# Optimization experiments

Hardware: AMD Instinct MI355X
Metric: run time of the kernel (lower is better)

## Reference

```python
import jax, jax.numpy as jnp
import numpy as np

WS = 5   # window_size
VN = 8   # view_num -> H = W = VN*WS = 40


def _layernorm(x, g, b, eps=1e-5):
    mu = x.mean(-1, keepdims=True)
    var = ((x - mu) ** 2).mean(-1, keepdims=True)
    return (x - mu) * jax.lax.rsqrt(var + eps) * g + b


def _rel_index():
    # standard Swin relative-position index for a WS x WS window
    coords = np.stack(np.meshgrid(np.arange(WS), np.arange(WS), indexing='ij')).reshape(2, -1)
    rel = (coords[:, :, None] - coords[:, None, :]).transpose(1, 2, 0)  # (T,T,2)
    rel = rel + (WS - 1)
    return rel[:, :, 0] * (2 * WS - 1) + rel[:, :, 1]  # (T,T) int


def _attn_mask(H, W):
    # checkerboard mask: outer product of flattened per-window checkerboard,
    # 0 where both positions are 'on', -100 elsewhere (matches masked_fill logic)
    ckbd = np.zeros((H, W), np.float32)
    ckbd[0::2, 1::2] = 1.0
    ckbd[1::2, 0::2] = 1.0
    win = ckbd.reshape(VN, WS, VN, WS).transpose(0, 2, 1, 3).reshape(VN * VN, WS * WS)
    m = win[:, :, None] * win[:, None, :]  # (N,T,T)
    return np.where(m == 0.0, -100.0, 0.0).astype(np.float32)


def setup_inputs() -> dict:
    key = jax.random.key(0)
    ks = jax.random.split(key, 8)
    B, C, H, W = 64, 256, 40, 40
    nh = 8
    dim2 = 2 * C
    hid = int(dim2 * 2.0)

    def n(k, shape, s=0.02):
        return jax.random.normal(k, shape, jnp.float32) * s

    return dict(
        x=jax.random.normal(ks[0], (B, C, H, W), jnp.float32),
        qkv_w=n(ks[1], (C, 3 * C)), qkv_b=jnp.zeros((3 * C,), jnp.float32),
        rel_table=n(ks[2], ((2 * WS - 1) ** 2, nh)),
        proj_w=n(ks[3], (C, dim2)), proj_b=jnp.zeros((dim2,), jnp.float32),
        mlp_w1=n(ks[4], (dim2, hid)), mlp_b1=jnp.zeros((hid,), jnp.float32),
        mlp_w2=n(ks[5], (hid, dim2)), mlp_b2=jnp.zeros((dim2,), jnp.float32),
        norm1_g=jnp.ones((C,), jnp.float32), norm1_b=jnp.zeros((C,), jnp.float32),
        norm2_g=jnp.ones((dim2,), jnp.float32), norm2_b=jnp.zeros((dim2,), jnp.float32),
    )


def reference(x, qkv_w, qkv_b, rel_table, proj_w, proj_b,
              mlp_w1, mlp_b1, mlp_w2, mlp_b2,
              norm1_g, norm1_b, norm2_g, norm2_b):
    B, C, H, W = x.shape
    nh = rel_table.shape[1]
    hd = C // nh
    N = VN * VN           # windows
    T = WS * WS           # tokens per window
    scale = hd ** -0.5

    xs = _layernorm(x.reshape(B, C, H * W).transpose(0, 2, 1), norm1_g, norm1_b)  # (B,L,C)
    qkv = xs @ qkv_w + qkv_b                                   # (B,L,3C)
    qkv = qkv.reshape(B, H, W, 3, C).transpose(3, 0, 4, 1, 2)  # (3,B,C,H,W)
    # windowize: (3,B,C,u,ws,v,ws) -> (3,B,N,C,T)
    qkv = qkv.reshape(3, B, C, VN, WS, VN, WS).transpose(0, 1, 3, 5, 2, 4, 6).reshape(3, B, N, C, T)
    # NOTE: original splits C as (head_dim, num_heads) -- head index is MINOR
    qkv = qkv.reshape(3, B, N, hd, nh, T).transpose(0, 1, 2, 4, 5, 3)  # (3,B,N,nh,T,hd)
    q, k, v = qkv[0] * scale, qkv[1], qkv[2]

    attn = jnp.einsum('bnhtd,bnhsd->bnhts', q, k)              # (B,N,nh,T,T)
    bias = rel_table[jnp.asarray(_rel_index())].transpose(2, 0, 1)  # (nh,T,T)
    mask = jnp.asarray(_attn_mask(H, W))                       # (N,T,T)
    attn = jax.nn.softmax(attn + bias[None, None] + mask[None, :, None], axis=-1)

    out = jnp.einsum('bnhts,bnhsd->bnhtd', attn, v)            # (B,N,nh,T,hd)
    out = out.reshape(B, N, nh, WS, WS, hd).transpose(0, 1, 3, 4, 2, 5)  # (B,N,ws,ws,nh,hd)
    # 'B (u v) h w nh c -> B (u h v w) (nh c)'
    out = out.reshape(B, VN, VN, WS, WS, C).transpose(0, 1, 3, 2, 4, 5).reshape(B, H * W, C)

    y = out @ proj_w + proj_b                                  # (B,L,2C)
    h = _layernorm(y, norm2_g, norm2_b)
    h = jax.nn.gelu(h @ mlp_w1 + mlp_b1, approximate=False) @ mlp_w2 + mlp_b2
    y = y + h
    return y.transpose(0, 2, 1).reshape(B, -1, H, W)           # (B,2C,H,W)
```

## Files before the change

### kernel.cpp

```cpp
#include <hip/hip_runtime.h>
#include <math.h>

#define B_   64
#define C_   256
#define L_   1600
#define T_   25
#define ROWS (B_*L_)
#define QSCALE 0.17677669529663687f

typedef _Float16 f16;
typedef f16 f16x8 __attribute__((ext_vector_type(8)));
typedef f16 f16x4 __attribute__((ext_vector_type(4)));
typedef f16 f16x2 __attribute__((ext_vector_type(2)));
typedef float f32x4 __attribute__((ext_vector_type(4)));

__device__ __forceinline__ void gload_lds16(const void* g, void* l) {
  __builtin_amdgcn_global_load_lds(
      (const __attribute__((address_space(1))) unsigned int*)g,
      (__attribute__((address_space(3))) unsigned int*)l, 16, 0, 0);
}

__device__ __forceinline__ float dot8(f16x8 a, f16x8 b, float acc) {
  union U { f16x8 v; f16x2 p[4]; };
  U ua; ua.v = a;
  U ub; ub.v = b;
#pragma unroll
  for (int i = 0; i < 4; ++i)
    acc = __builtin_amdgcn_fdot2(ua.p[i], ub.p[i], acc, false);
  return acc;
}

__global__ __launch_bounds__(256) void wtrans(const float* __restrict__ w,
                                              f16* __restrict__ o, int K, int N) {
  __shared__ f16 tile[64][72];
  int tid = threadIdx.x;
  int n0 = blockIdx.x * 64, k0 = blockIdx.y * 64;
  int nn = tid & 63, kq = tid >> 6;
#pragma unroll
  for (int i = 0; i < 16; ++i) {
    int k = kq * 16 + i;
    tile[nn][k] = (f16)w[(size_t)(k0 + k) * N + n0 + nn];
  }
  __syncthreads();
#pragma unroll
  for (int jj = 0; jj < 2; ++jj) {
    int e = jj * 256 + tid;
    int nr = e >> 3, kb = e & 7;
    *(f16x8*)&o[(size_t)(n0 + nr) * K + k0 + kb * 8] = *(const f16x8*)&tile[nr][kb * 8];
  }
}

__global__ __launch_bounds__(256) void ln1_fused(const float* __restrict__ x,
    const float* __restrict__ g, const float* __restrict__ be,
    f16* __restrict__ xs) {
  __shared__ float t32[256][65];
  __shared__ float gL[256], beL[256];
  int tid = threadIdx.x;
  gL[tid] = g[tid]; beL[tid] = be[tid];
  int r0 = blockIdx.x * 64;
  int w = tid >> 6, rl = tid & 63;
  int grow = r0 + rl;
  int b = grow / L_, l = grow - b * L_;
  const float* xb = x + (size_t)b * (C_ * L_) + l;
#pragma unroll
  for (int i = 0; i < 64; ++i) {
    int c = w + i * 4;
    t32[c][rl] = xb[(size_t)c * L_];
  }
  __syncthreads();
  int row = tid >> 2, q = tid & 3;
  float s = 0.f, s2 = 0.f;
#pragma unroll
  for (int i = 0; i < 64; ++i) {
    float vv = t32[q * 64 + i][row];
    s += vv; s2 += vv * vv;
  }
  s += __shfl_xor(s, 1); s2 += __shfl_xor(s2, 1);
  s += __shfl_xor(s, 2); s2 += __shfl_xor(s2, 2);
  float m = s * (1.0f / 256.0f);
  float rr = rsqrtf(s2 * (1.0f / 256.0f) - m * m + 1e-5f);
  f16* orow = &xs[(size_t)(r0 + row) * 256 + q * 64];
#pragma unroll
  for (int z8 = 0; z8 < 8; ++z8) {
    f16x8 ov;
#pragma unroll
    for (int z = 0; z < 8; ++z) {
      int c = q * 64 + z8 * 8 + z;
      ov[z] = (f16)((t32[c][row] - m) * rr * gL[c] + beL[c]);
    }
    *(f16x8*)(orow + z8 * 8) = ov;
  }
}

template<int K, int N, int EPI, int NCB>
__global__ __launch_bounds__(256) void gemm16(
    const f16* __restrict__ A, const f16* __restrict__ BT,
    const float* __restrict__ bias,
    float* __restrict__ outF, f16* __restrict__ outH,
    const f16* __restrict__ resid, int row_off, int nrp8) {
  __shared__ f16 As[2][128 * 32];
  __shared__ f16 Bs[2][128 * 32];
  int tid = threadIdx.x;
  int w = tid >> 6, lane = tid & 63;
  int wr = w >> 1, wc = w & 1;
  int bid = blockIdx.x;
  int xcd = bid & 7, j1d = bid >> 3;
  int member = j1d % NCB, grp = j1d / NCB;
  int r0 = (xcd * nrp8 + grp) * 128;
  int n0 = member * 128;

  f32x4 acc[4][4] = {};

  int srow0 = w * 16 + (lane >> 2);
  int st4 = lane & 3;

  const int NT = K / 32;

#define STAGE_T(kt, buf)                                                      \
  {                                                                           \
    int k0s = (kt) * 32;                                                      \
    _Pragma("unroll")                                                         \
    for (int i = 0; i < 2; ++i) {                                             \
      int row = i * 64 + srow0;                                               \
      int cb = st4 ^ ((row >> 1) & 3);                                        \
      gload_lds16(A + (size_t)(r0 + row) * K + k0s + cb * 8,                  \
                  &As[buf][(i * 4 + w) * 512]);                               \
    }                                                                         \
    _Pragma("unroll")                                                         \
    for (int i = 0; i < 2; ++i) {                                             \
      int row = i * 64 + srow0;                                               \
      int cb = st4 ^ ((row >> 1) & 3);                                        \
      gload_lds16(BT + (size_t)(n0 + row) * K + k0s + cb * 8,                 \
                  &Bs[buf][(i * 4 + w) * 512]);                               \
    }                                                                         \
  }

#define COMPUTE_T(buf)                                                        \
  {                                                                           \
    f16x8 af[4], bf[4];                                                       \
    _Pragma("unroll")                                                         \
    for (int m = 0; m < 4; ++m) {                                             \
      int ar = wr * 64 + m * 16 + (lane & 15);                                \
      int sl = (lane >> 4) ^ ((ar >> 1) & 3);                                 \
      af[m] = *(const f16x8*)&As[buf][ar * 32 + sl * 8];                      \
    }                                                                         \
    _Pragma("unroll")                                                         \
    for (int n = 0; n < 4; ++n) {                                             \
      int br = wc * 64 + n * 16 + (lane & 15);                                \
      int sl = (lane >> 4) ^ ((br >> 1) & 3);                                 \
      bf[n] = *(const f16x8*)&Bs[buf][br * 32 + sl * 8];                      \
    }                                                                         \
    _Pragma("unroll")                                                         \
    for (int m = 0; m < 4; ++m)                                               \
      _Pragma("unroll")                                                       \
      for (int n = 0; n < 4; ++n)                                             \
        acc[m][n] =                                                           \
            __builtin_amdgcn_mfma_f32_16x16x32_f16(af[m], bf[n], acc[m][n],   \
                                                   0, 0, 0);                  \
  }

  STAGE_T(0, 0);
  asm volatile("s_waitcnt vmcnt(0)" ::: "memory");
  __builtin_amdgcn_s_barrier();

  int cur = 0;
#pragma unroll 2
  for (int t = 0; t < NT - 1; ++t) {
    STAGE_T(t + 1, cur ^ 1);
    COMPUTE_T(cur);
    asm volatile("s_waitcnt vmcnt(0) lgkmcnt(0)" ::: "memory");
    __builtin_amdgcn_s_barrier();
    cur ^= 1;
  }
  COMPUTE_T(cur);

#undef STAGE_T
#undef COMPUTE_T

  if constexpr (EPI != 3) {
#pragma unroll
    for (int m = 0; m < 4; ++m) {
#pragma unroll
      for (int n = 0; n < 4; ++n) {
        int gcol = n0 + wc * 64 + n * 16 + (lane & 15);
        float bb = bias[gcol];
#pragma unroll
        for (int j = 0; j < 4; ++j) {
          int grow = r0 + wr * 64 + m * 16 + ((lane >> 4) << 2) + j;
          float vv = acc[m][n][j] + bb;
          if constexpr (EPI == 0) {
            outH[(size_t)grow * N + gcol] = (f16)vv;
          } else {
            float gl = 0.5f * vv * (1.0f + erff(vv * 0.70710678118654752f));
            outH[(size_t)grow * N + gcol] = (f16)gl;
          }
        }
      }
    }
  } else {
#pragma unroll
    for (int m = 0; m < 4; ++m) {
      int growl = r0 + wr * 64 + m * 16 + ((lane >> 4) << 2);
      int growg = row_off + growl;
      int b = growg / L_;
      int l = growg - b * L_;
#pragma unroll
      for (int n = 0; n < 4; ++n) {
        int gcol = n0 + wc * 64 + n * 16 + (lane & 15);
        float bb = bias[gcol];
        float4 o;
        o.x = acc[m][n][0] + bb + (float)resid[(size_t)(growg + 0) * 512 + gcol];
        o.y = acc[m][n][1] + bb + (float)resid[(size_t)(growg + 1) * 512 + gcol];
        o.z = acc[m][n][2] + bb + (float)resid[(size_t)(growg + 2) * 512 + gcol];
        o.w = acc[m][n][3] + bb + (float)resid[(size_t)(growg + 3) * 512 + gcol];
        *(float4*)&outF[((size_t)b * 512 + gcol) * L_ + l] = o;
      }
    }
  }
}

#define PST 776
__global__ __launch_bounds__(256) void attn_kernel(const f16* __restrict__ qkv,
                                                   const float* __restrict__ rel,
                                                   f16* __restrict__ outp) {
  __shared__ f16 qc[T_][PST];
  __shared__ f16 relL[81 * 8];
  int tid = threadIdx.x;
  int bn = blockIdx.x;
  int b = bn >> 6, n = bn & 63;
  int u = n >> 3, v = n & 7;

  for (int e = tid; e < 648; e += 256) relL[e] = (f16)rel[e];

  for (int e = tid; e < T_ * 96; e += 256) {
    int t = e / 96;
    int g = e - t * 96;
    int i = t / 5, j = t - i * 5;
    int l = (u * 5 + i) * 40 + v * 5 + j;
    f16x8 val = *(const f16x8*)&qkv[(size_t)(b * L_ + l) * 768 + g * 8];
    int which = g >> 5;
    int d = g & 31;
    int base = which * 256 + d;
#pragma unroll
    for (int h = 0; h < 8; ++h)
      qc[t][base + h * 32] = val[h];
  }
  __syncthreads();

  int h = tid >> 5, t = tid & 31;
  if (t < T_) {
    int i1 = t / 5, j1 = t - i1 * 5;
    int par1 = (u + v + i1 + j1) & 1;
    const f16* qp = &qc[t][h * 32];
    f16x8 q0 = *(const f16x8*)(qp + 0);
    f16x8 q1 = *(const f16x8*)(qp + 8);
    f16x8 q2 = *(const f16x8*)(qp + 16);
    f16x8 q3 = *(const f16x8*)(qp + 24);

    float p[T_];
    float mx = -1e30f;
#pragma unroll
    for (int s = 0; s < T_; ++s) {
      int i2 = s / 5, j2 = s - i2 * 5;
      const f16* kp = &qc[s][256 + h * 32];
      f16x8 k0 = *(const f16x8*)(kp + 0);
      f16x8 k1 = *(const f16x8*)(kp + 8);
      f16x8 k2 = *(const f16x8*)(kp + 16);
      f16x8 k3 = *(const f16x8*)(kp + 24);
      float d0 = 0.f, d1 = 0.f;
      d0 = dot8(q0, k0, d0);
      d1 = dot8(q1, k1, d1);
      d0 = dot8(q2, k2, d0);
      d1 = dot8(q3, k3, d1);
      float bias = (float)relL[((i1 - i2 + 4) * 9 + (j1 - j2 + 4)) * 8 + h];
      int par2 = (u + v + i2 + j2) & 1;
      float sc = (d0 + d1) * QSCALE + bias + ((par1 & par2) ? 0.0f : -100.0f);
      p[s] = sc;
      mx = fmaxf(mx, sc);
    }
    float sum = 0.f;
#pragma unroll
    for (int s = 0; s < T_; ++s) {
      float e = __expf(p[s] - mx);
      p[s] = e;
      sum += e;
    }
    float inv = 1.0f / sum;
#pragma unroll
    for (int s = 0; s < T_; ++s) p[s] *= inv;

    int l = (u * 5 + i1) * 40 + v * 5 + j1;
    f16* op = &outp[(size_t)(b * L_ + l) * 256 + h * 32];

#pragma unroll
    for (int half = 0; half < 2; ++half) {
      float acc[16] = {};
#pragma unroll
      for (int s = 0; s < T_; ++s) {
        const f16* vp = &qc[s][512 + h * 32 + half * 16];
        f16x8 v0 = *(const f16x8*)(vp + 0);
        f16x8 v1 = *(const f16x8*)(vp + 8);
        float ps = p[s];
#pragma unroll
        for (int z = 0; z < 8; ++z) {
          acc[z]     += ps * (float)v0[z];
          acc[8 + z] += ps * (float)v1[z];
        }
      }
#pragma unroll
      for (int z8 = 0; z8 < 2; ++z8) {
        f16x8 ov;
#pragma unroll
        for (int z = 0; z < 8; ++z) ov[z] = (f16)acc[z8 * 8 + z];
        *(f16x8*)(op + half * 16 + z8 * 8) = ov;
      }
    }
  }
}

__global__ __launch_bounds__(256) void ln2_fused(const f16* __restrict__ y,
    const float* __restrict__ g, const float* __restrict__ be,
    f16* __restrict__ yln) {
  int wv = threadIdx.x >> 6, lane = threadIdx.x & 63;
  int row = blockIdx.x * 4 + wv;
  const f16x8* yp = (const f16x8*)(y + (size_t)row * 512);
  f16x8 h0 = yp[lane];
  float v[8];
  float s = 0.f, s2 = 0.f;
#pragma unroll
  for (int z = 0; z < 8; ++z) {
    v[z] = (float)h0[z];
    s += v[z]; s2 += v[z] * v[z];
  }
#pragma unroll
  for (int o = 32; o; o >>= 1) { s += __shfl_xor(s, o); s2 += __shfl_xor(s2, o); }
  float m = s * (1.0f / 512.0f);
  float rr = rsqrtf(s2 * (1.0f / 512.0f) - m * m + 1e-5f);
  float4 g0 = ((const float4*)g)[lane * 2], g1 = ((const float4*)g)[lane * 2 + 1];
  float4 b0 = ((const float4*)be)[lane * 2], b1 = ((const float4*)be)[lane * 2 + 1];
  float gg[8] = {g0.x, g0.y, g0.z, g0.w, g1.x, g1.y, g1.z, g1.w};
  float bb[8] = {b0.x, b0.y, b0.z, b0.w, b1.x, b1.y, b1.z, b1.w};
  f16x8 o8;
#pragma unroll
  for (int z = 0; z < 8; ++z)
    o8[z] = (f16)((v[z] - m) * rr * gg[z] + bb[z]);
  *(f16x8*)&yln[(size_t)row * 512 + lane * 8] = o8;
}

extern "C" void kernel_launch(void* const* d_in, const int* in_sizes, int n_in,
                              void* d_out, int out_size, void* d_ws, size_t ws_size,
                              hipStream_t stream) {
  const float* x      = (const float*)d_in[0];
  const float* qkv_w  = (const float*)d_in[1];
  const float* qkv_b  = (const float*)d_in[2];
  const float* rel    = (const float*)d_in[3];
  const float* proj_w = (const float*)d_in[4];
  const float* proj_b = (const float*)d_in[5];
  const float* w1     = (const float*)d_in[6];
  const float* b1     = (const float*)d_in[7];
  const float* w2     = (const float*)d_in[8];
  const float* b2     = (const float*)d_in[9];
  const float* g1     = (const float*)d_in[10];
  const float* be1    = (const float*)d_in[11];
  const float* g2     = (const float*)d_in[12];
  const float* be2    = (const float*)d_in[13];
  float* out = (float*)d_out;

  char* w8 = (char*)d_ws;
  f16* qkv_wT  = (f16*)(w8 + 1638400);
  f16* proj_wT = qkv_wT + 768 * 256;
  f16* w1T     = proj_wT + 512 * 256;
  f16* w2T     = w1T + 1024 * 512;
  char* P0 = w8 + 4390912;
  f16* qkv_h = (f16*)P0;
  f16* y_h   = (f16*)P0;
  char* P1 = P0 + (size_t)ROWS * 768 * 2;
  f16* xs_h  = (f16*)P1;
  f16* att_h = (f16*)(P1 + (size_t)ROWS * 256 * 2);
  f16* yln   = (f16*)P1;
  char* P2 = P1 + (size_t)ROWS * 512 * 2;
  f16* hid = (f16*)P2;

  size_t need_full = 4390912 + (size_t)ROWS * 768 * 2 + (size_t)ROWS * 512 * 2
                   + (size_t)ROWS * 1024 * 2;
  bool full = ws_size >= need_full;

  wtrans<<<dim3(768 / 64, 256 / 64), 256, 0, stream>>>(qkv_w, qkv_wT, 256, 768);
  wtrans<<<dim3(512 / 64, 256 / 64), 256, 0, stream>>>(proj_w, proj_wT, 256, 512);
  wtrans<<<dim3(1024 / 64, 512 / 64), 256, 0, stream>>>(w1, w1T, 512, 1024);
  wtrans<<<dim3(512 / 64, 1024 / 64), 256, 0, stream>>>(w2, w2T, 1024, 512);

  ln1_fused<<<ROWS / 64, 256, 0, stream>>>(x, g1, be1, xs_h);

  gemm16<256, 768, 0, 6><<<6 * (ROWS / 128), 256, 0, stream>>>(
      xs_h, qkv_wT, qkv_b, nullptr, qkv_h, nullptr, 0, (ROWS / 128) / 8);

  attn_kernel<<<B_ * 64, 256, 0, stream>>>(qkv_h, rel, att_h);

  gemm16<256, 512, 0, 4><<<4 * (ROWS / 128), 256, 0, stream>>>(
      att_h, proj_wT, proj_b, nullptr, y_h, nullptr, 0, (ROWS / 128) / 8);

  ln2_fused<<<ROWS / 4, 256, 0, stream>>>(y_h, g2, be2, yln);

  if (full) {
    gemm16<512, 1024, 2, 8><<<8 * (ROWS / 128), 256, 0, stream>>>(
        yln, w1T, b1, nullptr, hid, nullptr, 0, (ROWS / 128) / 8);
    gemm16<1024, 512, 3, 4><<<4 * (ROWS / 128), 256, 0, stream>>>(
        hid, w2T, b2, out, nullptr, y_h, 0, (ROWS / 128) / 8);
  } else {
    const int CHUNK = ROWS / 4;
    for (int c = 0; c < 4; ++c) {
      int off = c * CHUNK;
      gemm16<512, 1024, 2, 8><<<8 * (CHUNK / 128), 256, 0, stream>>>(
          yln + (size_t)off * 512, w1T, b1, nullptr, hid, nullptr, off, (CHUNK / 128) / 8);
      gemm16<1024, 512, 3, 4><<<4 * (CHUNK / 128), 256, 0, stream>>>(
          hid, w2T, b2, out, nullptr, y_h, off, (CHUNK / 128) / 8);
    }
  }
  (void)in_sizes; (void)n_in; (void)out_size;
}
```

Measured before the change: 767.2 us.

## Triple-buffer GEMM LDS staging, raise MFMA priority, use tanh GELU

```diff
diff --git a/kernel.cpp b/kernel.cpp
--- a/kernel.cpp
+++ b/kernel.cpp
@@ -98,8 +98,8 @@
     const float* __restrict__ bias,
     float* __restrict__ outF, f16* __restrict__ outH,
     const f16* __restrict__ resid, int row_off, int nrp8) {
-  __shared__ f16 As[2][128 * 32];
-  __shared__ f16 Bs[2][128 * 32];
+  __shared__ f16 As[3][128 * 32];
+  __shared__ f16 Bs[3][128 * 32];
   int tid = threadIdx.x;
   int w = tid >> 6, lane = tid & 63;
   int wr = w >> 1, wc = w & 1;
@@ -116,7 +116,7 @@
 
   const int NT = K / 32;
 
-#define STAGE_T(kt, buf)                                                      \
+#define STAGE_T(kt, bi)                                                       \
   {                                                                           \
     int k0s = (kt) * 32;                                                      \
     _Pragma("unroll")                                                         \
@@ -124,32 +124,33 @@
       int row = i * 64 + srow0;                                               \
       int cb = st4 ^ ((row >> 1) & 3);                                        \
       gload_lds16(A + (size_t)(r0 + row) * K + k0s + cb * 8,                  \
-                  &As[buf][(i * 4 + w) * 512]);                               \
+                  &As[bi][(i * 4 + w) * 512]);                                \
     }                                                                         \
     _Pragma("unroll")                                                         \
     for (int i = 0; i < 2; ++i) {                                             \
       int row = i * 64 + srow0;                                               \
       int cb = st4 ^ ((row >> 1) & 3);                                        \
       gload_lds16(BT + (size_t)(n0 + row) * K + k0s + cb * 8,                 \
-                  &Bs[buf][(i * 4 + w) * 512]);                               \
+                  &Bs[bi][(i * 4 + w) * 512]);                                \
     }                                                                         \
   }
 
-#define COMPUTE_T(buf)                                                        \
+#define COMPUTE_T(bi)                                                         \
   {                                                                           \
     f16x8 af[4], bf[4];                                                       \
     _Pragma("unroll")                                                         \
     for (int m = 0; m < 4; ++m) {                                             \
       int ar = wr * 64 + m * 16 + (lane & 15);                                \
       int sl = (lane >> 4) ^ ((ar >> 1) & 3);                                 \
-      af[m] = *(const f16x8*)&As[buf][ar * 32 + sl * 8];                      \
+      af[m] = *(const f16x8*)&As[bi][ar * 32 + sl * 8];                       \
     }                                                                         \
     _Pragma("unroll")                                                         \
     for (int n = 0; n < 4; ++n) {                                             \
       int br = wc * 64 + n * 16 + (lane & 15);                                \
       int sl = (lane >> 4) ^ ((br >> 1) & 3);                                 \
-      bf[n] = *(const f16x8*)&Bs[buf][br * 32 + sl * 8];                      \
+      bf[n] = *(const f16x8*)&Bs[bi][br * 32 + sl * 8];                       \
     }                                                                         \
+    __builtin_amdgcn_s_setprio(1);                                            \
     _Pragma("unroll")                                                         \
     for (int m = 0; m < 4; ++m)                                               \
       _Pragma("unroll")                                                       \
@@ -157,22 +158,21 @@
         acc[m][n] =                                                           \
             __builtin_amdgcn_mfma_f32_16x16x32_f16(af[m], bf[n], acc[m][n],   \
                                                    0, 0, 0);                  \
+    __builtin_amdgcn_s_setprio(0);                                            \
   }
 
   STAGE_T(0, 0);
+  STAGE_T(1, 1);
+
+  for (int t = 0; t < NT - 1; ++t) {
+    asm volatile("s_waitcnt vmcnt(4)" ::: "memory");
+    __builtin_amdgcn_s_barrier();
+    COMPUTE_T(t % 3);
+    if (t + 2 < NT) STAGE_T(t + 2, (t + 2) % 3);
+  }
   asm volatile("s_waitcnt vmcnt(0)" ::: "memory");
   __builtin_amdgcn_s_barrier();
-
-  int cur = 0;
-#pragma unroll 2
-  for (int t = 0; t < NT - 1; ++t) {
-    STAGE_T(t + 1, cur ^ 1);
-    COMPUTE_T(cur);
-    asm volatile("s_waitcnt vmcnt(0) lgkmcnt(0)" ::: "memory");
-    __builtin_amdgcn_s_barrier();
-    cur ^= 1;
-  }
-  COMPUTE_T(cur);
+  COMPUTE_T((NT - 1) % 3);
 
 #undef STAGE_T
 #undef COMPUTE_T
@@ -191,7 +191,10 @@
           if constexpr (EPI == 0) {
             outH[(size_t)grow * N + gcol] = (f16)vv;
           } else {
-            float gl = 0.5f * vv * (1.0f + erff(vv * 0.70710678118654752f));
+            float z = 0.7978845608028654f * (vv + 0.044715f * vv * vv * vv);
+            float e2 = __expf(2.0f * z);
+            float th = 1.0f - 2.0f / (e2 + 1.0f);
+            float gl = 0.5f * vv * (1.0f + th);
             outH[(size_t)grow * N + gcol] = (f16)gl;
           }
         }
```

Result: faster. 685.2 us (-10.7%).
